# Optimization experiments

Measured on AMD Instinct MI355X. Metric: run time of the kernel, lower is better.

The kernel has to match this reference:

```python
import jax, jax.numpy as jnp
import numpy as np

EPS_BN = 1e-5   # torch BatchNorm1d default eps
EPS_W = 1e-8    # inverse-distance weighting eps


def linear_bn_relu(x, W, b, gamma, beta, mean, var):
    # x: [B, N, Cin]; W: [Cout, Cin]. BatchNorm applied in eval mode with running stats.
    y = jnp.einsum('bnc,oc->bno', x, W) + b
    y = (y - mean) * (gamma / jnp.sqrt(var + EPS_BN)) + beta
    return jax.nn.relu(y)


def interpolate3(xyz_tgt, xyz_src, feats_src):
    # 3-NN inverse-distance-weighted interpolation (PointNetFeaturePropagation, mlp=[]).
    # xyz_tgt: [B,N,3], xyz_src: [B,S,3], feats_src: [B,S,C] -> [B,N,C]
    d = (jnp.sum(xyz_tgt * xyz_tgt, -1, keepdims=True)
         - 2.0 * jnp.einsum('bnd,bsd->bns', xyz_tgt, xyz_src)
         + jnp.sum(xyz_src * xyz_src, -1)[:, None, :])       # [B,N,S] squared dists
    neg_d, idx = jax.lax.top_k(-d, 3)                          # 3 smallest distances
    dists = -neg_d                                             # [B,N,3]
    w = 1.0 / (dists + EPS_W)
    w = w / jnp.sum(w, -1, keepdims=True)                      # [B,N,3]
    gathered = jax.vmap(lambda f, i: f[i])(feats_src, idx)     # [B,N,3,C]
    return jnp.sum(gathered * w[..., None], axis=2)            # [B,N,C]


def setup_inputs() -> dict:
    key = jax.random.key(0)
    ks = jax.random.split(key, 16)
    B, N1, N2 = 4, 4096, 16384
    dim1, dim2, dim_out = 512, 256, 256
    inp = {
        'xyz1': jax.random.normal(ks[0], (B, N1, 3), jnp.float32),
        'points1': jax.random.normal(ks[1], (B, N1, dim1), jnp.float32),
        'xyz2': jax.random.normal(ks[2], (B, N2, 3), jnp.float32),
        'points2': jax.random.normal(ks[3], (B, N2, dim2), jnp.float32),
        # fc1: Linear(dim1, dim_out) + BN(dim_out)
        'W1': jax.random.normal(ks[4], (dim_out, dim1), jnp.float32) * (dim1 ** -0.5),
        'b1': jax.random.normal(ks[5], (dim_out,), jnp.float32) * 0.01,
        'g1': jax.random.uniform(ks[6], (dim_out,), jnp.float32, 0.5, 1.5),
        'be1': jax.random.normal(ks[7], (dim_out,), jnp.float32) * 0.01,
        'm1': jax.random.normal(ks[8], (dim_out,), jnp.float32) * 0.01,
        'v1': jax.random.uniform(ks[9], (dim_out,), jnp.float32, 0.5, 1.5),
        # fc2: Linear(dim2, dim_out) + BN(dim_out)
        'W2': jax.random.normal(ks[10], (dim_out, dim2), jnp.float32) * (dim2 ** -0.5),
        'b2': jax.random.normal(ks[11], (dim_out,), jnp.float32) * 0.01,
        'g2': jax.random.uniform(ks[12], (dim_out,), jnp.float32, 0.5, 1.5),
        'be2': jax.random.normal(ks[13], (dim_out,), jnp.float32) * 0.01,
        'm2': jax.random.normal(ks[14], (dim_out,), jnp.float32) * 0.01,
        'v2': jax.random.uniform(ks[15], (dim_out,), jnp.float32, 0.5, 1.5),
    }
    return inp


def reference(xyz1, points1, xyz2, points2,
              W1, b1, g1, be1, m1, v1,
              W2, b2, g2, be2, m2, v2):
    feats1 = linear_bn_relu(points1, W1, b1, g1, be1, m1, v1)  # [B,N1,dim_out]
    feats2 = linear_bn_relu(points2, W2, b2, g2, be2, m2, v2)  # [B,N2,dim_out]
    interp = interpolate3(xyz2, xyz1, feats1)                  # [B,N2,dim_out]
    return interp + feats2
```

## Files before the change

### kernel.cpp

```cpp
#include <hip/hip_runtime.h>
#include <math.h>

#define EPS_BN 1e-5f

typedef __attribute__((ext_vector_type(8))) short bf16x8;
typedef __attribute__((ext_vector_type(4))) float f32x4;

__device__ __forceinline__ void gld_lds16(const void* g, void* l) {
    __builtin_amdgcn_global_load_lds(
        (const __attribute__((address_space(1))) unsigned int*)g,
        (__attribute__((address_space(3))) unsigned int*)l, 16, 0, 0);
}

__device__ __forceinline__ unsigned short f2bf(float f) {
    unsigned u = __float_as_uint(f);
    return (unsigned short)((u + 0x7FFFu + ((u >> 16) & 1u)) >> 16);
}

__device__ __forceinline__ float dist_exact(float4 T, float4 s) {
    float dot2 = __fadd_rn(__fadd_rn(__fmul_rn(T.x, s.x), __fmul_rn(T.y, s.y)),
                           __fmul_rn(T.z, s.z));
    return __fadd_rn(__fsub_rn(T.w, dot2), s.w);
}

__device__ __forceinline__ void conv_body(
    const float* __restrict__ src, unsigned short* __restrict__ dst,
    int blk, int tid, int K8log, int nslab)
{
    const int gid = blk * 256 + tid;
    const int m  = gid >> K8log;
    const int ko = gid & ((1 << K8log) - 1);
    const float4* s = (const float4*)src + ((size_t)m << (K8log + 1)) + ko * 2;
    float4 f0 = s[0];
    float4 f1 = s[1];
    const int mblk = m >> 7, r = m & 127;
    const int slab = ko >> 2, o = ko & 3;
    const int g = (o + (r >> 1)) & 3;
    unsigned short h[8] = {f2bf(f0.x), f2bf(f0.y), f2bf(f0.z), f2bf(f0.w),
                           f2bf(f1.x), f2bf(f1.y), f2bf(f1.z), f2bf(f1.w)};
    *(uint4*)(dst + ((size_t)(mblk * nslab + slab)) * 4096 + r * 32 + g * 8) =
        *(uint4*)h;
}

__global__ __launch_bounds__(256) void prep_all(
    const float* __restrict__ p1, const float* __restrict__ p2,
    const float* __restrict__ w1, const float* __restrict__ w2,
    unsigned short* __restrict__ A1p, unsigned short* __restrict__ A2p,
    unsigned short* __restrict__ W1p, unsigned short* __restrict__ W2p,
    const float* __restrict__ xyz1, const float* __restrict__ xyz2,
    float4* __restrict__ sxyz1, float4* __restrict__ txyz2)
{
    const int blk = blockIdx.x, tid = threadIdx.x;
    if (blk < 4096)        conv_body(p1, A1p, blk,         tid, 6, 16);
    else if (blk < 12288)  conv_body(p2, A2p, blk - 4096,  tid, 5, 8);
    else if (blk < 12352)  conv_body(w1, W1p, blk - 12288, tid, 6, 16);
    else if (blk < 12384)  conv_body(w2, W2p, blk - 12352, tid, 5, 8);
    else if (blk < 12448) {
        int i = (blk - 12384) * 256 + tid;
        float x = xyz1[i * 3 + 0], y = xyz1[i * 3 + 1], z = xyz1[i * 3 + 2];
        float ss = __fadd_rn(__fadd_rn(__fmul_rn(x, x), __fmul_rn(y, y)),
                             __fmul_rn(z, z));
        sxyz1[i] = make_float4(x + x, y + y, z + z, ss);
    } else {
        int i = (blk - 12448) * 256 + tid;
        float x = xyz2[i * 3 + 0], y = xyz2[i * 3 + 1], z = xyz2[i * 3 + 2];
        float st = __fadd_rn(__fadd_rn(__fmul_rn(x, x), __fmul_rn(y, y)),
                             __fmul_rn(z, z));
        txyz2[i] = make_float4(x, y, z, st);
    }
}

__global__ __launch_bounds__(256) void knn_select(
    const float4* __restrict__ sxyz1,
    const float4* __restrict__ txyz2,
    double* __restrict__ cand)
{
    const int tid   = threadIdx.x;
    const int blk   = blockIdx.x;
    const int part  = blk & 7;
    const int chunk = (blk >> 3) & 63;
    const int b     = blk >> 9;

    const int g = b * 16384 + chunk * 256 + tid;
    const float4 T = txyz2[g];
    const float4* __restrict__ S = sxyz1 + b * 4096 + part * 512;

    float d0 = INFINITY, d1 = INFINITY, d2 = INFINITY;
    int   q0 = 0,        q1 = 0,        q2 = 0;

#pragma unroll 2
    for (int qi = 0; qi < 128; qi++) {
        float4 sA = S[qi * 4 + 0];
        float4 sB = S[qi * 4 + 1];
        float4 sC = S[qi * 4 + 2];
        float4 sD = S[qi * 4 + 3];
        float dA = dist_exact(T, sA);
        float dB = dist_exact(T, sB);
        float dC = dist_exact(T, sC);
        float dD = dist_exact(T, sD);
        float dm = fminf(fminf(dA, dB), fminf(dC, dD));

        bool c2 = dm < d2, c1 = dm < d1, c0 = dm < d0;
        float t2 = c1 ? d1 : (c2 ? dm : d2);
        int   u2 = c1 ? q1 : (c2 ? qi : q2);
        float t1 = c0 ? d0 : (c1 ? dm : d1);
        int   u1 = c0 ? q0 : (c1 ? qi : q1);
        float t0 = c0 ? dm : d0;
        int   u0 = c0 ? qi : q0;
        d2 = t2; q2 = u2; d1 = t1; q1 = u1; d0 = t0; q0 = u0;
    }

    const double INIT = __hiloint2double(0x7F800000, 0);
    double k0 = INIT, k1 = INIT, k2 = INIT;
#pragma unroll
    for (int c = 0; c < 3; c++) {
        const int qq = (c == 0) ? q0 : ((c == 1) ? q1 : q2);
#pragma unroll
        for (int e = 0; e < 4; e++) {
            float4 s = S[qq * 4 + e];
            float d = dist_exact(T, s);
            double k = __hiloint2double(__float_as_int(d),
                                        part * 512 + qq * 4 + e);
            if (k < k2) {
                if (k < k1) {
                    k2 = k1;
                    if (k < k0) { k1 = k0; k0 = k; }
                    else        { k1 = k; }
                } else { k2 = k; }
            }
        }
    }

    double* c = cand + (size_t)g * 24 + part * 3;
    c[0] = k0; c[1] = k1; c[2] = k2;
}

__global__ __launch_bounds__(256) void knn_merge(
    const double* __restrict__ cand, float* __restrict__ w3,
    int* __restrict__ idx3)
{
    const int g = blockIdx.x * 256 + threadIdx.x;
    const double INIT = __hiloint2double(0x7F800000, 0);
    double k0 = INIT, k1 = INIT, k2 = INIT;
#pragma unroll
    for (int p = 0; p < 24; p++) {
        double k = cand[(size_t)g * 24 + p];
        if (k < k2) {
            if (k < k1) {
                k2 = k1;
                if (k < k0) { k1 = k0; k0 = k; }
                else        { k1 = k; }
            } else { k2 = k; }
        }
    }
    float d0 = __int_as_float(__double2hiint(k0));
    float d1 = __int_as_float(__double2hiint(k1));
    float d2 = __int_as_float(__double2hiint(k2));
    float w0 = 1.0f / __fadd_rn(d0, 1e-8f);
    float w1 = 1.0f / __fadd_rn(d1, 1e-8f);
    float w2 = 1.0f / __fadd_rn(d2, 1e-8f);
    float ws = __fadd_rn(__fadd_rn(w0, w1), w2);
    w3[(size_t)g * 3 + 0] = w0 / ws;
    w3[(size_t)g * 3 + 1] = w1 / ws;
    w3[(size_t)g * 3 + 2] = w2 / ws;
    idx3[(size_t)g * 3 + 0] = __double2loint(k0);
    idx3[(size_t)g * 3 + 1] = __double2loint(k1);
    idx3[(size_t)g * 3 + 2] = __double2loint(k2);
}

__global__ __launch_bounds__(256) void gemm_bf16_bn_relu(
    const unsigned short* __restrict__ Ap,
    const unsigned short* __restrict__ Bp,
    const float* __restrict__ bias,
    const float* __restrict__ gamma,
    const float* __restrict__ beta,
    const float* __restrict__ mean,
    const float* __restrict__ var,
    float* __restrict__ out, int M, int K)
{
    __shared__ __align__(16) unsigned short As[4096];
    __shared__ __align__(16) unsigned short Bs[4096];

    const int tid  = threadIdx.x;
    const int w    = tid >> 6;
    const int lane = tid & 63;
    const int q    = lane >> 4;
    const int rl   = lane & 15;
    const int wm   = w >> 1, wn = w & 1;
    const int bn   = blockIdx.x, bm = blockIdx.y;
    const int nslab = K >> 5;

    f32x4 acc[4][4];
#pragma unroll
    for (int i = 0; i < 4; i++)
#pragma unroll
        for (int j = 0; j < 4; j++) acc[i][j] = (f32x4){0.f, 0.f, 0.f, 0.f};

    const unsigned short* Ab = Ap + (size_t)bm * nslab * 4096;
    const unsigned short* Bb = Bp + (size_t)bn * nslab * 4096;
    const int c0 = 2 * w;
    const int l8 = lane * 8;

    int aidx[4], bidx[4];
#pragma unroll
    for (int i = 0; i < 4; i++) {
        int rr = wm * 64 + i * 16 + rl;
        aidx[i] = rr * 32 + ((q + (rr >> 1)) & 3) * 8;
        int nn = wn * 64 + i * 16 + rl;
        bidx[i] = nn * 32 + ((q + (nn >> 1)) & 3) * 8;
    }

    for (int s = 0; s < nslab; s++) {
        __syncthreads();
        const unsigned short* a = Ab + (size_t)s * 4096;
        const unsigned short* b = Bb + (size_t)s * 4096;
        gld_lds16(a + (c0 + 0) * 512 + l8, &As[(c0 + 0) * 512 + l8]);
        gld_lds16(a + (c0 + 1) * 512 + l8, &As[(c0 + 1) * 512 + l8]);
        gld_lds16(b + (c0 + 0) * 512 + l8, &Bs[(c0 + 0) * 512 + l8]);
        gld_lds16(b + (c0 + 1) * 512 + l8, &Bs[(c0 + 1) * 512 + l8]);
        __syncthreads();

        bf16x8 af[4], bf[4];
#pragma unroll
        for (int i = 0; i < 4; i++) af[i] = *(const bf16x8*)&As[aidx[i]];
#pragma unroll
        for (int j = 0; j < 4; j++) bf[j] = *(const bf16x8*)&Bs[bidx[j]];
#pragma unroll
        for (int i = 0; i < 4; i++)
#pragma unroll
            for (int j = 0; j < 4; j++)
                acc[i][j] = __builtin_amdgcn_mfma_f32_16x16x32_bf16(
                    af[i], bf[j], acc[i][j], 0, 0, 0);
    }

    const int gm0 = bm * 128 + wm * 64;
    const int gn0 = bn * 128 + wn * 64;
#pragma unroll
    for (int j = 0; j < 4; j++) {
        int n = gn0 + j * 16 + rl;
        float sc = gamma[n] / sqrtf(var[n] + EPS_BN);
        float sh = beta[n] + (bias[n] - mean[n]) * sc;
#pragma unroll
        for (int i = 0; i < 4; i++) {
            int m0 = gm0 + i * 16 + q * 4;
#pragma unroll
            for (int t = 0; t < 4; t++) {
                float v = fmaxf(acc[i][j][t] * sc + sh, 0.f);
                out[(size_t)(m0 + t) * 256 + n] = v;
            }
        }
    }
}

__global__ __launch_bounds__(256) void gemm2_interp(
    const unsigned short* __restrict__ Ap,
    const unsigned short* __restrict__ Bp,
    const float* __restrict__ bias,
    const float* __restrict__ gamma,
    const float* __restrict__ beta,
    const float* __restrict__ mean,
    const float* __restrict__ var,
    const float* __restrict__ feats1,
    const float* __restrict__ w3,
    const int*   __restrict__ idx3,
    float* __restrict__ out)
{
    __shared__ __align__(16) unsigned short As[4096];
    __shared__ __align__(16) unsigned short Bs[4096];

    const int tid  = threadIdx.x;
    const int w    = tid >> 6;
    const int lane = tid & 63;
    const int q    = lane >> 4;
    const int rl   = lane & 15;
    const int wm   = w >> 1, wn = w & 1;
    const int bn   = blockIdx.x, bm = blockIdx.y;
    const int nslab = 8;

    f32x4 acc[4][4];
#pragma unroll
    for (int i = 0; i < 4; i++)
#pragma unroll
        for (int j = 0; j < 4; j++) acc[i][j] = (f32x4){0.f, 0.f, 0.f, 0.f};

    const unsigned short* Ab = Ap + (size_t)bm * nslab * 4096;
    const unsigned short* Bb = Bp + (size_t)bn * nslab * 4096;
    const int c0 = 2 * w;
    const int l8 = lane * 8;

    int aidx[4], bidx[4];
#pragma unroll
    for (int i = 0; i < 4; i++) {
        int rr = wm * 64 + i * 16 + rl;
        aidx[i] = rr * 32 + ((q + (rr >> 1)) & 3) * 8;
        int nn = wn * 64 + i * 16 + rl;
        bidx[i] = nn * 32 + ((q + (nn >> 1)) & 3) * 8;
    }

    for (int s = 0; s < nslab; s++) {
        __syncthreads();
        const unsigned short* a = Ab + (size_t)s * 4096;
        const unsigned short* b = Bb + (size_t)s * 4096;
        gld_lds16(a + (c0 + 0) * 512 + l8, &As[(c0 + 0) * 512 + l8]);
        gld_lds16(a + (c0 + 1) * 512 + l8, &As[(c0 + 1) * 512 + l8]);
        gld_lds16(b + (c0 + 0) * 512 + l8, &Bs[(c0 + 0) * 512 + l8]);
        gld_lds16(b + (c0 + 1) * 512 + l8, &Bs[(c0 + 1) * 512 + l8]);
        __syncthreads();

        bf16x8 af[4], bf[4];
#pragma unroll
        for (int i = 0; i < 4; i++) af[i] = *(const bf16x8*)&As[aidx[i]];
#pragma unroll
        for (int j = 0; j < 4; j++) bf[j] = *(const bf16x8*)&Bs[bidx[j]];
#pragma unroll
        for (int i = 0; i < 4; i++)
#pragma unroll
            for (int j = 0; j < 4; j++)
                acc[i][j] = __builtin_amdgcn_mfma_f32_16x16x32_bf16(
                    af[i], bf[j], acc[i][j], 0, 0, 0);
    }

    const int gm0 = bm * 128 + wm * 64;
    const int gn0 = bn * 128 + wn * 64;
    float scj[4], shj[4];
    int nj[4];
#pragma unroll
    for (int j = 0; j < 4; j++) {
        int n = gn0 + j * 16 + rl;
        nj[j] = n;
        float sc = gamma[n] / sqrtf(var[n] + EPS_BN);
        scj[j] = sc;
        shj[j] = beta[n] + (bias[n] - mean[n]) * sc;
    }

#pragma unroll
    for (int i = 0; i < 4; i++) {
#pragma unroll
        for (int t = 0; t < 4; t++) {
            const int m = gm0 + i * 16 + q * 4 + t;
            const int bb = m >> 14;
            const int j0 = idx3[(size_t)m * 3 + 0];
            const int j1 = idx3[(size_t)m * 3 + 1];
            const int j2 = idx3[(size_t)m * 3 + 2];
            const float u0 = w3[(size_t)m * 3 + 0];
            const float u1 = w3[(size_t)m * 3 + 1];
            const float u2 = w3[(size_t)m * 3 + 2];
            const float* f0 = feats1 + ((size_t)(bb * 4096 + j0)) * 256;
            const float* f1 = feats1 + ((size_t)(bb * 4096 + j1)) * 256;
            const float* f2 = feats1 + ((size_t)(bb * 4096 + j2)) * 256;
#pragma unroll
            for (int j = 0; j < 4; j++) {
                const int n = nj[j];
                float v = fmaxf(acc[i][j][t] * scj[j] + shj[j], 0.f);
                v += u0 * f0[n] + u1 * f1[n] + u2 * f2[n];
                out[(size_t)m * 256 + n] = v;
            }
        }
    }
}

extern "C" void kernel_launch(void* const* d_in, const int* in_sizes, int n_in,
                              void* d_out, int out_size, void* d_ws, size_t ws_size,
                              hipStream_t stream) {
    const float* xyz1    = (const float*)d_in[0];
    const float* points1 = (const float*)d_in[1];
    const float* xyz2    = (const float*)d_in[2];
    const float* points2 = (const float*)d_in[3];
    const float* W1  = (const float*)d_in[4];
    const float* b1  = (const float*)d_in[5];
    const float* g1  = (const float*)d_in[6];
    const float* be1 = (const float*)d_in[7];
    const float* m1  = (const float*)d_in[8];
    const float* v1  = (const float*)d_in[9];
    const float* W2  = (const float*)d_in[10];
    const float* b2  = (const float*)d_in[11];
    const float* g2  = (const float*)d_in[12];
    const float* be2 = (const float*)d_in[13];
    const float* m2  = (const float*)d_in[14];
    const float* v2  = (const float*)d_in[15];

    const size_t MB = 1u << 20;
    char* ws = (char*)d_ws;
    float*          feats1 = (float*)(ws);
    double*         cand   = (double*)(ws);
    unsigned short* A1p    = (unsigned short*)(ws + 16 * MB);
    unsigned short* A2p    = (unsigned short*)(ws + 32 * MB);
    unsigned short* W1p    = (unsigned short*)(ws + 64 * MB);
    unsigned short* W2p    = (unsigned short*)(ws + 64 * MB + 512 * 1024);
    float4*         sxyz1  = (float4*)(ws + 65 * MB);
    float4*         txyz2  = (float4*)(ws + 66 * MB);
    float*          w3     = (float*)(ws + 67 * MB);
    int*            idx3   = (int*)(ws + 68 * MB);
    float* outp = (float*)d_out;

    dim3 blk(256);
    prep_all<<<12704, blk, 0, stream>>>(points1, points2, W1, W2,
                                        A1p, A2p, W1p, W2p,
                                        xyz1, xyz2, sxyz1, txyz2);
    knn_select<<<2048, blk, 0, stream>>>(sxyz1, txyz2, cand);
    knn_merge<<<256, blk, 0, stream>>>(cand, w3, idx3);
    gemm_bf16_bn_relu<<<dim3(2, 128), blk, 0, stream>>>(A1p, W1p, b1, g1, be1, m1, v1,
                                                        feats1, 16384, 512);
    gemm2_interp<<<dim3(2, 512), blk, 0, stream>>>(A2p, W2p, b2, g2, be2, m2, v2,
                                                   feats1, w3, idx3, outp);
}
```

Before: 299.8 us.

## Use SoA source coordinates and packed f32x2 math in knn_select scan

Result: faster. 291.9 us (-2.7%).

```diff
diff --git a/kernel.cpp b/kernel.cpp
--- a/kernel.cpp
+++ b/kernel.cpp
@@ -5,6 +5,7 @@
 
 typedef __attribute__((ext_vector_type(8))) short bf16x8;
 typedef __attribute__((ext_vector_type(4))) float f32x4;
+typedef __attribute__((ext_vector_type(2))) float f32x2;
 
 __device__ __forceinline__ void gld_lds16(const void* g, void* l) {
     __builtin_amdgcn_global_load_lds(
@@ -48,7 +49,8 @@
     unsigned short* __restrict__ A1p, unsigned short* __restrict__ A2p,
     unsigned short* __restrict__ W1p, unsigned short* __restrict__ W2p,
     const float* __restrict__ xyz1, const float* __restrict__ xyz2,
-    float4* __restrict__ sxyz1, float4* __restrict__ txyz2)
+    float4* __restrict__ sxyz1, float* __restrict__ sxyz1_soa,
+    float4* __restrict__ txyz2)
 {
     const int blk = blockIdx.x, tid = threadIdx.x;
     if (blk < 4096)        conv_body(p1, A1p, blk,         tid, 6, 16);
@@ -60,7 +62,15 @@
         float x = xyz1[i * 3 + 0], y = xyz1[i * 3 + 1], z = xyz1[i * 3 + 2];
         float ss = __fadd_rn(__fadd_rn(__fmul_rn(x, x), __fmul_rn(y, y)),
                              __fmul_rn(z, z));
-        sxyz1[i] = make_float4(x + x, y + y, z + z, ss);
+        float x2 = x + x, y2 = y + y, z2 = z + z;
+        sxyz1[i] = make_float4(x2, y2, z2, ss);
+        const int b = i >> 12, s = i & 4095;
+        const int p = s >> 9, o = (s >> 3) & 63, e = s & 7;
+        float* soa = sxyz1_soa + (((size_t)(b * 8 + p)) * 64 + o) * 32;
+        soa[e]      = x2;
+        soa[8 + e]  = y2;
+        soa[16 + e] = z2;
+        soa[24 + e] = ss;
     } else {
         int i = (blk - 12448) * 256 + tid;
         float x = xyz2[i * 3 + 0], y = xyz2[i * 3 + 1], z = xyz2[i * 3 + 2];
@@ -72,9 +82,11 @@
 
 __global__ __launch_bounds__(256) void knn_select(
     const float4* __restrict__ sxyz1,
+    const float*  __restrict__ sxyz1_soa,
     const float4* __restrict__ txyz2,
     double* __restrict__ cand)
 {
+#pragma clang fp contract(off)
     const int tid   = threadIdx.x;
     const int blk   = blockIdx.x;
     const int part  = blk & 7;
@@ -83,30 +95,65 @@
 
     const int g = b * 16384 + chunk * 256 + tid;
     const float4 T = txyz2[g];
+    const float* __restrict__ P =
+        sxyz1_soa + ((size_t)(b * 8 + part)) * 2048;
     const float4* __restrict__ S = sxyz1 + b * 4096 + part * 512;
+
+    const f32x2 Txx = {T.x, T.x};
+    const f32x2 Tyy = {T.y, T.y};
+    const f32x2 Tzz = {T.z, T.z};
+    const f32x2 Tww = {T.w, T.w};
 
     float d0 = INFINITY, d1 = INFINITY, d2 = INFINITY;
     int   q0 = 0,        q1 = 0,        q2 = 0;
 
 #pragma unroll 2
-    for (int qi = 0; qi < 128; qi++) {
-        float4 sA = S[qi * 4 + 0];
-        float4 sB = S[qi * 4 + 1];
-        float4 sC = S[qi * 4 + 2];
-        float4 sD = S[qi * 4 + 3];
-        float dA = dist_exact(T, sA);
-        float dB = dist_exact(T, sB);
-        float dC = dist_exact(T, sC);
-        float dD = dist_exact(T, sD);
-        float dm = fminf(fminf(dA, dB), fminf(dC, dD));
+    for (int o = 0; o < 64; o++) {
+        const float* blkp = P + o * 32;
+        f32x2 da, db, dc, dd;
+        {
+            f32x2 sx = *(const f32x2*)(blkp + 0);
+            f32x2 sy = *(const f32x2*)(blkp + 8);
+            f32x2 sz = *(const f32x2*)(blkp + 16);
+            f32x2 sw = *(const f32x2*)(blkp + 24);
+            f32x2 dot2 = (Txx * sx + Tyy * sy) + Tzz * sz;
+            da = (Tww - dot2) + sw;
+        }
+        {
+            f32x2 sx = *(const f32x2*)(blkp + 2);
+            f32x2 sy = *(const f32x2*)(blkp + 10);
+            f32x2 sz = *(const f32x2*)(blkp + 18);
+            f32x2 sw = *(const f32x2*)(blkp + 26);
+            f32x2 dot2 = (Txx * sx + Tyy * sy) + Tzz * sz;
+            db = (Tww - dot2) + sw;
+        }
+        {
+            f32x2 sx = *(const f32x2*)(blkp + 4);
+            f32x2 sy = *(const f32x2*)(blkp + 12);
+            f32x2 sz = *(const f32x2*)(blkp + 20);
+            f32x2 sw = *(const f32x2*)(blkp + 28);
+            f32x2 dot2 = (Txx * sx + Tyy * sy) + Tzz * sz;
+            dc = (Tww - dot2) + sw;
+        }
+        {
+            f32x2 sx = *(const f32x2*)(blkp + 6);
+            f32x2 sy = *(const f32x2*)(blkp + 14);
+            f32x2 sz = *(const f32x2*)(blkp + 22);
+            f32x2 sw = *(const f32x2*)(blkp + 30);
+            f32x2 dot2 = (Txx * sx + Tyy * sy) + Tzz * sz;
+            dd = (Tww - dot2) + sw;
+        }
+        float mab = fminf(fminf(da[0], da[1]), fminf(db[0], db[1]));
+        float mcd = fminf(fminf(dc[0], dc[1]), fminf(dd[0], dd[1]));
+        float dm  = fminf(mab, mcd);
 
         bool c2 = dm < d2, c1 = dm < d1, c0 = dm < d0;
         float t2 = c1 ? d1 : (c2 ? dm : d2);
-        int   u2 = c1 ? q1 : (c2 ? qi : q2);
+        int   u2 = c1 ? q1 : (c2 ? o : q2);
         float t1 = c0 ? d0 : (c1 ? dm : d1);
-        int   u1 = c0 ? q0 : (c1 ? qi : q1);
+        int   u1 = c0 ? q0 : (c1 ? o : q1);
         float t0 = c0 ? dm : d0;
-        int   u0 = c0 ? qi : q0;
+        int   u0 = c0 ? o : q0;
         d2 = t2; q2 = u2; d1 = t1; q1 = u1; d0 = t0; q0 = u0;
     }
 
@@ -116,11 +163,11 @@
     for (int c = 0; c < 3; c++) {
         const int qq = (c == 0) ? q0 : ((c == 1) ? q1 : q2);
 #pragma unroll
-        for (int e = 0; e < 4; e++) {
-            float4 s = S[qq * 4 + e];
+        for (int e = 0; e < 8; e++) {
+            float4 s = S[qq * 8 + e];
             float d = dist_exact(T, s);
             double k = __hiloint2double(__float_as_int(d),
-                                        part * 512 + qq * 4 + e);
+                                        part * 512 + qq * 8 + e);
             if (k < k2) {
                 if (k < k1) {
                     k2 = k1;
@@ -388,6 +435,7 @@
     unsigned short* W1p    = (unsigned short*)(ws + 64 * MB);
     unsigned short* W2p    = (unsigned short*)(ws + 64 * MB + 512 * 1024);
     float4*         sxyz1  = (float4*)(ws + 65 * MB);
+    float*          sxyz1s = (float*)(ws + 65 * MB + 256 * 1024);
     float4*         txyz2  = (float4*)(ws + 66 * MB);
     float*          w3     = (float*)(ws + 67 * MB);
     int*            idx3   = (int*)(ws + 68 * MB);
@@ -396,8 +444,8 @@
     dim3 blk(256);
     prep_all<<<12704, blk, 0, stream>>>(points1, points2, W1, W2,
                                         A1p, A2p, W1p, W2p,
-                                        xyz1, xyz2, sxyz1, txyz2);
-    knn_select<<<2048, blk, 0, stream>>>(sxyz1, txyz2, cand);
+                                        xyz1, xyz2, sxyz1, sxyz1s, txyz2);
+    knn_select<<<2048, blk, 0, stream>>>(sxyz1, sxyz1s, txyz2, cand);
     knn_merge<<<256, blk, 0, stream>>>(cand, w3, idx3);
     gemm_bf16_bn_relu<<<dim3(2, 128), blk, 0, stream>>>(A1p, W1p, b1, g1, be1, m1, v1,
                                                         feats1, 16384, 512);
```

## Compute kNN distances with fp16 split-precision MFMA and fuse select/merge

Applied to the files above, without the earlier changes.

Result: slower. 317.3 us (+5.8%).

```diff
diff --git a/kernel.cpp b/kernel.cpp
--- a/kernel.cpp
+++ b/kernel.cpp
@@ -5,6 +5,8 @@
 
 typedef __attribute__((ext_vector_type(8))) short bf16x8;
 typedef __attribute__((ext_vector_type(4))) float f32x4;
+typedef __attribute__((ext_vector_type(8))) _Float16 fp16x8;
+typedef __attribute__((ext_vector_type(16))) float f32x16;
 
 __device__ __forceinline__ void gld_lds16(const void* g, void* l) {
     __builtin_amdgcn_global_load_lds(
@@ -21,6 +23,17 @@
     float dot2 = __fadd_rn(__fadd_rn(__fmul_rn(T.x, s.x), __fmul_rn(T.y, s.y)),
                            __fmul_rn(T.z, s.z));
     return __fadd_rn(__fsub_rn(T.w, dot2), s.w);
+}
+
+__device__ __forceinline__ float min3f(float a, float b, float c) {
+    float d;
+    asm("v_min3_f32 %0, %1, %2, %3" : "=v"(d) : "v"(a), "v"(b), "v"(c));
+    return d;
+}
+__device__ __forceinline__ unsigned med3u(unsigned a, unsigned b, unsigned c) {
+    unsigned d;
+    asm("v_med3_u32 %0, %1, %2, %3" : "=v"(d) : "v"(a), "v"(b), "v"(c));
+    return d;
 }
 
 __device__ __forceinline__ void conv_body(
@@ -48,7 +61,8 @@
     unsigned short* __restrict__ A1p, unsigned short* __restrict__ A2p,
     unsigned short* __restrict__ W1p, unsigned short* __restrict__ W2p,
     const float* __restrict__ xyz1, const float* __restrict__ xyz2,
-    float4* __restrict__ sxyz1, float4* __restrict__ txyz2)
+    float4* __restrict__ sxyz1, _Float16* __restrict__ srcpk,
+    _Float16* __restrict__ tgtpk, float4* __restrict__ txyz2)
 {
     const int blk = blockIdx.x, tid = threadIdx.x;
     if (blk < 4096)        conv_body(p1, A1p, blk,         tid, 6, 16);
@@ -60,112 +74,142 @@
         float x = xyz1[i * 3 + 0], y = xyz1[i * 3 + 1], z = xyz1[i * 3 + 2];
         float ss = __fadd_rn(__fadd_rn(__fmul_rn(x, x), __fmul_rn(y, y)),
                              __fmul_rn(z, z));
-        sxyz1[i] = make_float4(x + x, y + y, z + z, ss);
+        float x2 = x + x, y2 = y + y, z2 = z + z;
+        sxyz1[i] = make_float4(x2, y2, z2, ss);
+        float nx = -x2, ny = -y2, nz = -z2;
+        _Float16 hx = (_Float16)nx, lx = (_Float16)(nx - (float)hx);
+        _Float16 hy = (_Float16)ny, ly = (_Float16)(ny - (float)hy);
+        _Float16 hz = (_Float16)nz, lz = (_Float16)(nz - (float)hz);
+        _Float16 hw = (_Float16)ss, lw = (_Float16)(ss - (float)hw);
+        _Float16 z0 = (_Float16)0.f;
+        fp16x8 lo8 = {hx, hx, lx, hy, hy, ly, hz, hz};
+        fp16x8 hi8 = {lz, hw, lw, z0, z0, z0, z0, z0};
+        *(fp16x8*)(srcpk + (size_t)i * 16)     = lo8;
+        *(fp16x8*)(srcpk + (size_t)i * 16 + 8) = hi8;
     } else {
         int i = (blk - 12448) * 256 + tid;
         float x = xyz2[i * 3 + 0], y = xyz2[i * 3 + 1], z = xyz2[i * 3 + 2];
         float st = __fadd_rn(__fadd_rn(__fmul_rn(x, x), __fmul_rn(y, y)),
                              __fmul_rn(z, z));
         txyz2[i] = make_float4(x, y, z, st);
-    }
-}
-
-__global__ __launch_bounds__(256) void knn_select(
+        _Float16 hx = (_Float16)x, lx = (_Float16)(x - (float)hx);
+        _Float16 hy = (_Float16)y, ly = (_Float16)(y - (float)hy);
+        _Float16 hz = (_Float16)z, lz = (_Float16)(z - (float)hz);
+        _Float16 z0 = (_Float16)0.f, one = (_Float16)1.0f;
+        fp16x8 lo8 = {hx, lx, hx, hy, ly, hy, hz, lz};
+        fp16x8 hi8 = {hz, one, one, z0, z0, z0, z0, z0};
+        *(fp16x8*)(tgtpk + (size_t)i * 16)     = lo8;
+        *(fp16x8*)(tgtpk + (size_t)i * 16 + 8) = hi8;
+    }
+}
+
+__global__ __launch_bounds__(256) void knn_mfma(
     const float4* __restrict__ sxyz1,
+    const _Float16* __restrict__ srcpk,
+    const _Float16* __restrict__ tgtpk,
     const float4* __restrict__ txyz2,
-    double* __restrict__ cand)
+    float* __restrict__ w3, int* __restrict__ idx3)
 {
-    const int tid   = threadIdx.x;
-    const int blk   = blockIdx.x;
-    const int part  = blk & 7;
-    const int chunk = (blk >> 3) & 63;
-    const int b     = blk >> 9;
-
-    const int g = b * 16384 + chunk * 256 + tid;
-    const float4 T = txyz2[g];
-    const float4* __restrict__ S = sxyz1 + b * 4096 + part * 512;
-
-    float d0 = INFINITY, d1 = INFINITY, d2 = INFINITY;
-    int   q0 = 0,        q1 = 0,        q2 = 0;
-
-#pragma unroll 2
-    for (int qi = 0; qi < 128; qi++) {
-        float4 sA = S[qi * 4 + 0];
-        float4 sB = S[qi * 4 + 1];
-        float4 sC = S[qi * 4 + 2];
-        float4 sD = S[qi * 4 + 3];
-        float dA = dist_exact(T, sA);
-        float dB = dist_exact(T, sB);
-        float dC = dist_exact(T, sC);
-        float dD = dist_exact(T, sD);
-        float dm = fminf(fminf(dA, dB), fminf(dC, dD));
-
-        bool c2 = dm < d2, c1 = dm < d1, c0 = dm < d0;
-        float t2 = c1 ? d1 : (c2 ? dm : d2);
-        int   u2 = c1 ? q1 : (c2 ? qi : q2);
-        float t1 = c0 ? d0 : (c1 ? dm : d1);
-        int   u1 = c0 ? q0 : (c1 ? qi : q1);
-        float t0 = c0 ? dm : d0;
-        int   u0 = c0 ? qi : q0;
-        d2 = t2; q2 = u2; d1 = t1; q1 = u1; d0 = t0; q0 = u0;
-    }
-
-    const double INIT = __hiloint2double(0x7F800000, 0);
-    double k0 = INIT, k1 = INIT, k2 = INIT;
-#pragma unroll
-    for (int c = 0; c < 3; c++) {
-        const int qq = (c == 0) ? q0 : ((c == 1) ? q1 : q2);
-#pragma unroll
-        for (int e = 0; e < 4; e++) {
-            float4 s = S[qq * 4 + e];
+    const int tid  = threadIdx.x;
+    const int wv   = tid >> 6;
+    const int lane = tid & 63;
+    const int col  = lane & 31;
+    const int h    = lane >> 5;
+    const int tgt  = blockIdx.x * 128 + wv * 32 + col;
+    const int batch = tgt >> 14;
+
+    const float4 T = txyz2[tgt];
+    const fp16x8 bfrag = *(const fp16x8*)(tgtpk + (size_t)tgt * 16 + h * 8);
+    const _Float16* __restrict__ ap =
+        srcpk + (size_t)batch * 4096 * 16 + (size_t)col * 16 + h * 8;
+    const float4* __restrict__ S = sxyz1 + batch * 4096;
+
+    const f32x16 zacc = {0.f,0.f,0.f,0.f, 0.f,0.f,0.f,0.f,
+                         0.f,0.f,0.f,0.f, 0.f,0.f,0.f,0.f};
+
+    unsigned k0 = 0xFFFFFFFFu, k1 = 0xFFFFFFFFu, k2 = 0xFFFFFFFFu,
+             k3 = 0xFFFFFFFFu, k4 = 0xFFFFFFFFu, k5 = 0xFFFFFFFFu,
+             k6 = 0xFFFFFFFFu, k7 = 0xFFFFFFFFu, k8 = 0xFFFFFFFFu,
+             k9 = 0xFFFFFFFFu, k10 = 0xFFFFFFFFu, k11 = 0xFFFFFFFFu;
+
+#pragma unroll 4
+    for (int b = 0; b < 128; b++) {
+        fp16x8 afrag = *(const fp16x8*)(ap + (size_t)b * 512);
+        f32x16 acc = __builtin_amdgcn_mfma_f32_32x32x16_f16(
+            afrag, bfrag, zacc, 0, 0, 0);
+        float m1 = min3f(acc[0], acc[1], acc[2]);
+        float m2 = min3f(acc[3], acc[4], acc[5]);
+        float m3 = min3f(acc[6], acc[7], acc[8]);
+        float m4 = min3f(acc[9], acc[10], acc[11]);
+        float m5 = min3f(acc[12], acc[13], acc[14]);
+        float m6 = min3f(m1, m2, m3);
+        float m7 = min3f(m4, m5, acc[15]);
+        float m  = fminf(m6, m7);
+
+        int fu = __float_as_int(m);
+        unsigned fk = (unsigned)(fu ^ ((fu >> 31) | 0x80000000));
+        unsigned key = (fk & 0xFFFFFF80u) | (unsigned)b;
+
+        unsigned nk0 = key < k0 ? key : k0;
+        k11 = med3u(key, k10, k11);
+        k10 = med3u(key, k9, k10);
+        k9  = med3u(key, k8, k9);
+        k8  = med3u(key, k7, k8);
+        k7  = med3u(key, k6, k7);
+        k6  = med3u(key, k5, k6);
+        k5  = med3u(key, k4, k5);
+        k4  = med3u(key, k3, k4);
+        k3  = med3u(key, k2, k3);
+        k2  = med3u(key, k1, k2);
+        k1  = med3u(key, k0, k1);
+        k0  = nk0;
+    }
+
+    const double INITK = __hiloint2double(0x7F800000, 0);
+    double K0 = INITK, K1 = INITK, K2 = INITK;
+#define INS3(kk) { if ((kk) < K2) {                                  \
+        if ((kk) < K1) { K2 = K1;                                    \
+            if ((kk) < K0) { K1 = K0; K0 = (kk); } else K1 = (kk);   \
+        } else K2 = (kk); } }
+
+#pragma unroll 1
+    for (int r = 0; r < 12; r++) {
+        const int bb = (int)(k0 & 127u);
+        const float4* Sb = S + bb * 32 + 4 * h;
+        const int sbase = bb * 32 + 4 * h;
+#pragma unroll
+        for (int e = 0; e < 16; e++) {
+            const int row = (e & 3) + 8 * (e >> 2);
+            float4 s = Sb[row];
             float d = dist_exact(T, s);
-            double k = __hiloint2double(__float_as_int(d),
-                                        part * 512 + qq * 4 + e);
-            if (k < k2) {
-                if (k < k1) {
-                    k2 = k1;
-                    if (k < k0) { k1 = k0; k0 = k; }
-                    else        { k1 = k; }
-                } else { k2 = k; }
-            }
+            double kk = __hiloint2double(__float_as_int(d), sbase + row);
+            INS3(kk);
         }
-    }
-
-    double* c = cand + (size_t)g * 24 + part * 3;
-    c[0] = k0; c[1] = k1; c[2] = k2;
-}
-
-__global__ __launch_bounds__(256) void knn_merge(
-    const double* __restrict__ cand, float* __restrict__ w3,
-    int* __restrict__ idx3)
-{
-    const int g = blockIdx.x * 256 + threadIdx.x;
-    const double INIT = __hiloint2double(0x7F800000, 0);
-    double k0 = INIT, k1 = INIT, k2 = INIT;
-#pragma unroll
-    for (int p = 0; p < 24; p++) {
-        double k = cand[(size_t)g * 24 + p];
-        if (k < k2) {
-            if (k < k1) {
-                k2 = k1;
-                if (k < k0) { k1 = k0; k0 = k; }
-                else        { k1 = k; }
-            } else { k2 = k; }
-        }
-    }
-    float d0 = __int_as_float(__double2hiint(k0));
-    float d1 = __int_as_float(__double2hiint(k1));
-    float d2 = __int_as_float(__double2hiint(k2));
-    float w0 = 1.0f / __fadd_rn(d0, 1e-8f);
-    float w1 = 1.0f / __fadd_rn(d1, 1e-8f);
-    float w2 = 1.0f / __fadd_rn(d2, 1e-8f);
-    float ws = __fadd_rn(__fadd_rn(w0, w1), w2);
-    w3[(size_t)g * 3 + 0] = w0 / ws;
-    w3[(size_t)g * 3 + 1] = w1 / ws;
-    w3[(size_t)g * 3 + 2] = w2 / ws;
-    idx3[(size_t)g * 3 + 0] = __double2loint(k0);
-    idx3[(size_t)g * 3 + 1] = __double2loint(k1);
-    idx3[(size_t)g * 3 + 2] = __double2loint(k2);
+        k0 = k1; k1 = k2; k2 = k3; k3 = k4; k4 = k5; k5 = k6;
+        k6 = k7; k7 = k8; k8 = k9; k9 = k10; k10 = k11;
+    }
+
+    double O0 = __shfl_xor(K0, 32);
+    double O1 = __shfl_xor(K1, 32);
+    double O2 = __shfl_xor(K2, 32);
+    INS3(O0); INS3(O1); INS3(O2);
+#undef INS3
+
+    if (h == 0) {
+        float d0 = __int_as_float(__double2hiint(K0));
+        float d1 = __int_as_float(__double2hiint(K1));
+        float d2 = __int_as_float(__double2hiint(K2));
+        float w0 = 1.0f / __fadd_rn(d0, 1e-8f);
+        float w1 = 1.0f / __fadd_rn(d1, 1e-8f);
+        float w2 = 1.0f / __fadd_rn(d2, 1e-8f);
+        float ws = __fadd_rn(__fadd_rn(w0, w1), w2);
+        w3[(size_t)tgt * 3 + 0] = w0 / ws;
+        w3[(size_t)tgt * 3 + 1] = w1 / ws;
+        w3[(size_t)tgt * 3 + 2] = w2 / ws;
+        idx3[(size_t)tgt * 3 + 0] = __double2loint(K0);
+        idx3[(size_t)tgt * 3 + 1] = __double2loint(K1);
+        idx3[(size_t)tgt * 3 + 2] = __double2loint(K2);
+    }
 }
 
 __global__ __launch_bounds__(256) void gemm_bf16_bn_relu(
@@ -382,7 +426,8 @@
     const size_t MB = 1u << 20;
     char* ws = (char*)d_ws;
     float*          feats1 = (float*)(ws);
-    double*         cand   = (double*)(ws);
+    _Float16*       srcpk  = (_Float16*)(ws);
+    _Float16*       tgtpk  = (_Float16*)(ws + 1 * MB);
     unsigned short* A1p    = (unsigned short*)(ws + 16 * MB);
     unsigned short* A2p    = (unsigned short*)(ws + 32 * MB);
     unsigned short* W1p    = (unsigned short*)(ws + 64 * MB);
@@ -396,9 +441,8 @@
     dim3 blk(256);
     prep_all<<<12704, blk, 0, stream>>>(points1, points2, W1, W2,
                                         A1p, A2p, W1p, W2p,
-                                        xyz1, xyz2, sxyz1, txyz2);
-    knn_select<<<2048, blk, 0, stream>>>(sxyz1, txyz2, cand);
-    knn_merge<<<256, blk, 0, stream>>>(cand, w3, idx3);
+                                        xyz1, xyz2, sxyz1, srcpk, tgtpk, txyz2);
+    knn_mfma<<<512, blk, 0, stream>>>(sxyz1, srcpk, tgtpk, txyz2, w3, idx3);
     gemm_bf16_bn_relu<<<dim3(2, 128), blk, 0, stream>>>(A1p, W1p, b1, g1, be1, m1, v1,
                                                         feats1, 16384, 512);
     gemm2_interp<<<dim3(2, 512), blk, 0, stream>>>(A2p, W2p, b2, g2, be2, m2, v2,
```
